# Optimization experiments

Measured on AMD Instinct MI355X. Metric: run time of the kernel, lower is better.

The kernel has to match this reference:

```python
import jax, jax.numpy as jnp
import numpy as np

B, N = 4, 2048
INPUT_DIM, KDIM, VDIM = 128, 128, 16
EMBED, V_EMBED, H = 128, 128, 8
HEAD_DIM = EMBED // H          # 16
V_HEAD_DIM = V_EMBED // H      # 16 (== VDIM, required by the torch view)
SCALING = HEAD_DIM ** -0.5


def setup_inputs() -> dict:
    key = jax.random.key(0)
    ks = jax.random.split(key, 12)
    inp = {
        "query": jax.random.normal(ks[0], (B, N, INPUT_DIM), dtype=jnp.float32),
        "key": jax.random.normal(ks[1], (B, N, KDIM), dtype=jnp.float32),
        "value": jax.random.normal(ks[2], (B, N, VDIM), dtype=jnp.float32),
        # nn.Linear weights are [out, in]; init.normal_ -> std normal
        "Wq": jax.random.normal(ks[3], (EMBED, INPUT_DIM), dtype=jnp.float32),
        "bq": jnp.zeros((EMBED,), dtype=jnp.float32),
        "Wk": jax.random.normal(ks[4], (EMBED, KDIM), dtype=jnp.float32),
        "bk": jnp.zeros((EMBED,), dtype=jnp.float32),
        "Wv": jax.random.normal(ks[5], (V_EMBED, VDIM), dtype=jnp.float32),
        "bv": jnp.zeros((V_EMBED,), dtype=jnp.float32),
        "Wo": jax.random.normal(ks[6], (V_EMBED // H, V_EMBED), dtype=jnp.float32),
        "bo": jnp.zeros((V_EMBED // H,), dtype=jnp.float32),
    }
    return inp


def reference(query, key, value, Wq, bq, Wk, bk, Wv, bv, Wo, bo):
    # projections
    q = (query @ Wq.T + bq) * SCALING                 # [B, N, EMBED]
    k = key @ Wk.T + bk                               # [B, N, EMBED]
    v = value @ Wv.T + bv                             # [B, N, V_EMBED]
    # split heads: [B, H, N, head_dim]
    q = q.reshape(B, N, H, HEAD_DIM).transpose(0, 2, 1, 3)
    k = k.reshape(B, N, H, HEAD_DIM).transpose(0, 2, 1, 3)
    v = v.reshape(B, N, H, V_HEAD_DIM).transpose(0, 2, 1, 3)
    # full NxN scores (naive attention, as in the source)
    scores = jnp.einsum("bhnd,bhmd->bhnm", q, k)      # [B, H, N, N]
    attn = jax.nn.softmax(scores, axis=-1)
    # dropout is identity in eval mode
    ctx = jnp.einsum("bhnm,bhme->bhne", attn, v)      # [B, H, N, V_HEAD_DIM]
    ctx = ctx.transpose(0, 2, 1, 3).reshape(B, N, V_EMBED)
    out = ctx @ Wo.T + bo                             # [B, N, V_EMBED // H]
    return out
```

## Files before the change

kernel.cpp:

```cpp
#include <hip/hip_runtime.h>
#include <hip/hip_bf16.h>
#include <math.h>

typedef unsigned short ushort_t;
typedef unsigned int uint_t;
typedef __bf16 bf16x8 __attribute__((ext_vector_type(8)));
typedef float f32x4 __attribute__((ext_vector_type(4)));
typedef __fp16 fp16v2 __attribute__((ext_vector_type(2)));
typedef _Float16 f16x4 __attribute__((ext_vector_type(4)));

#define NSEQ 2048
#define QSCALE 0.3606737602222409f

__device__ __forceinline__ float exp2_fast(float x) {
#if __has_builtin(__builtin_amdgcn_exp2f)
    return __builtin_amdgcn_exp2f(x);
#else
    return exp2f(x);
#endif
}

union U8 { ushort_t u[8]; bf16x8 v; uint4 q; uint_t w[4]; };
union F8 { float f[8]; float4 v4[2]; };
union H4 { fp16v2 h2[2]; f16x4 v; uint_t w[2]; };
union HV { fp16v2 h2[4]; uint4 q; };

__device__ __forceinline__ uint_t pk2(float a, float b) {
    __hip_bfloat162 h2 = __float22bfloat162_rn(make_float2(a, b));
    union { __hip_bfloat162 h; uint_t u; } cv; cv.h = h2; return cv.u;
}

__device__ __forceinline__ void split8(const F8& x, U8& hi, U8& lo) {
#pragma unroll
    for (int p = 0; p < 4; ++p) {
        const float a = x.f[2*p], b = x.f[2*p+1];
        const uint_t hw = pk2(a, b);
        hi.w[p] = hw;
        const float ha = __uint_as_float(hw << 16);
        const float hb = __uint_as_float(hw & 0xFFFF0000u);
        lo.w[p] = pk2(a - ha, b - hb);
    }
}

__global__ __launch_bounds__(256) void wpack_kernel(
    const float* __restrict__ Wq, const float* __restrict__ Wk,
    const float* __restrict__ Wo,
    ushort_t* __restrict__ wpk_hi, ushort_t* __restrict__ wpk_lo,
    ushort_t* __restrict__ wo_hi, ushort_t* __restrict__ wo_lo)
{
    const int idx = blockIdx.x * 256 + threadIdx.x;
    if (idx < 4096) {
        const int lane = idx & 63;
        const int f    = (idx >> 6) & 3;
        const int ct   = (idx >> 8) & 7;
        const int mat  = idx >> 11;
        const float* W = mat ? Wk : Wq;
        const float* src = W + (size_t)(ct * 16 + (lane & 15)) * 128
                             + f * 32 + (lane >> 4) * 8;
        F8 x; x.v4[0] = *(const float4*)src; x.v4[1] = *(const float4*)(src + 4);
        U8 hi, lo;
        split8(x, hi, lo);
        const size_t dst = (size_t)mat * 16384 + ((size_t)(ct * 4 + f) * 64 + lane) * 8;
        *(uint4*)(wpk_hi + dst) = hi.q;
        *(uint4*)(wpk_lo + dst) = lo.q;
    } else if (idx < 4352) {
        const int i2   = idx - 4096;
        const int lane = i2 & 63;
        const int f    = i2 >> 6;
        const float* src = Wo + (size_t)(lane & 15) * 128
                              + f * 32 + (lane >> 4) * 8;
        F8 x; x.v4[0] = *(const float4*)src; x.v4[1] = *(const float4*)(src + 4);
        U8 hi, lo;
        split8(x, hi, lo);
        const size_t dst = ((size_t)f * 64 + lane) * 8;
        *(uint4*)(wo_hi + dst) = hi.q;
        *(uint4*)(wo_lo + dst) = lo.q;
    }
}

__global__ __launch_bounds__(256, 2) void proj_kernel(
    const float* __restrict__ query, const float* __restrict__ key,
    const float* __restrict__ value,
    const float* __restrict__ bq, const float* __restrict__ bk,
    const float* __restrict__ Wv, const float* __restrict__ bv,
    const ushort_t* __restrict__ wpk_hi, const ushort_t* __restrict__ wpk_lo,
    ushort_t* __restrict__ q_hi, ushort_t* __restrict__ q_lo,
    ushort_t* __restrict__ k_hi, ushort_t* __restrict__ k_lo,
    ushort_t* __restrict__ vt)
{
    const int t   = threadIdx.x;
    const int w   = t >> 6;
    const int l   = t & 63;
    const int col = l & 15;
    const int g   = l >> 4;
    const int rbase = blockIdx.x * 16;
    const int b = rbase >> 11;

    const int isK    = w >> 1;
    const int cthalf = (w & 1) * 4;

    const float* X = isK ? key : query;
    const float* xrow = X + (size_t)(rbase + col) * 128 + g * 8;
    bf16x8 xh[4], xl[4];
#pragma unroll
    for (int f = 0; f < 4; ++f) {
        F8 x;
        x.v4[0] = *(const float4*)(xrow + f * 32);
        x.v4[1] = *(const float4*)(xrow + f * 32 + 4);
        U8 hi, lo;
        split8(x, hi, lo);
        xh[f] = hi.v; xl[f] = lo.v;
    }

    const float* bias = isK ? bk : bq;
    ushort_t* dhi = isK ? k_hi : q_hi;
    ushort_t* dlo = isK ? k_lo : q_lo;
    const float scale = isK ? 1.0f : QSCALE;
    const int tok = (rbase & 2047) + col;

#pragma unroll
    for (int ctl = 0; ctl < 4; ++ctl) {
        const int h = cthalf + ctl;
        bf16x8 whf[4], wlf[4];
#pragma unroll
        for (int f = 0; f < 4; ++f) {
            const size_t o = (size_t)isK * 16384
                           + ((size_t)(h * 4 + f) * 64 + l) * 8;
            whf[f] = *(const bf16x8*)(wpk_hi + o);
            wlf[f] = *(const bf16x8*)(wpk_lo + o);
        }
        const float4 b4 = *(const float4*)(bias + h * 16 + 4 * g);
        f32x4 acc = {b4.x, b4.y, b4.z, b4.w};
#pragma unroll
        for (int f = 0; f < 4; ++f) {
            acc = __builtin_amdgcn_mfma_f32_16x16x32_bf16(whf[f], xh[f], acc, 0, 0, 0);
            acc = __builtin_amdgcn_mfma_f32_16x16x32_bf16(wlf[f], xh[f], acc, 0, 0, 0);
            acc = __builtin_amdgcn_mfma_f32_16x16x32_bf16(whf[f], xl[f], acc, 0, 0, 0);
        }
        const size_t abase = ((size_t)(b * 8 + h) * NSEQ + tok) * 16 + 4 * g;
        const float a0 = acc[0]*scale, a1 = acc[1]*scale;
        const float a2 = acc[2]*scale, a3 = acc[3]*scale;
        const uint_t h01 = pk2(a0, a1), h23 = pk2(a2, a3);
        const uint_t l01 = pk2(a0 - __uint_as_float(h01 << 16),
                               a1 - __uint_as_float(h01 & 0xFFFF0000u));
        const uint_t l23 = pk2(a2 - __uint_as_float(h23 << 16),
                               a3 - __uint_as_float(h23 & 0xFFFF0000u));
        uint2 sh; sh.x = h01; sh.y = h23;
        uint2 sl; sl.x = l01; sl.y = l23;
        *(uint2*)(dhi + abase) = sh;
        *(uint2*)(dlo + abase) = sl;
    }

    const int e  = t & 127;
    const int rh = t >> 7;
    const int r0 = rbase + rh * 8;
    const float4* Wv4 = (const float4*)(Wv + (size_t)e * 16);
    const float4 wv0 = Wv4[0], wv1 = Wv4[1], wv2 = Wv4[2], wv3 = Wv4[3];
    const float bvv = bv[e];
    F8 af;
#pragma unroll
    for (int r = 0; r < 8; ++r) {
        const float4* xv4 = (const float4*)(value + (size_t)(r0 + r) * 16);
        const float4 x0 = xv4[0], x1 = xv4[1], x2 = xv4[2], x3 = xv4[3];
        float a = bvv;
        a += wv0.x*x0.x + wv0.y*x0.y + wv0.z*x0.z + wv0.w*x0.w;
        a += wv1.x*x1.x + wv1.y*x1.y + wv1.z*x1.z + wv1.w*x1.w;
        a += wv2.x*x2.x + wv2.y*x2.y + wv2.z*x2.z + wv2.w*x2.w;
        a += wv3.x*x3.x + wv3.y*x3.y + wv3.z*x3.z + wv3.w*x3.w;
        af.f[r] = a;
    }
    HV vpk;
#pragma unroll
    for (int p = 0; p < 4; ++p)
        vpk.h2[p] = __builtin_amdgcn_cvt_pkrtz(af.f[2*p], af.f[2*p+1]);
    const int hv = e >> 4, dd = e & 15;
    *(uint4*)(vt + ((size_t)(b * 8 + hv) * 16 + dd) * NSEQ + (r0 & 2047)) = vpk.q;
}

__global__ __launch_bounds__(256, 4) void attn_kernel(
    const ushort_t* __restrict__ q_hi, const ushort_t* __restrict__ q_lo,
    const ushort_t* __restrict__ k_hi, const ushort_t* __restrict__ k_lo,
    const ushort_t* __restrict__ vt, ushort_t* __restrict__ ctxb)
{
    const int t    = threadIdx.x;
    const int w    = t >> 6;
    const int l    = t & 63;
    const int col  = l & 15;
    const int g    = l >> 4;
    const int qsub = w & 1;
    const int kh   = w >> 1;

    const int id   = blockIdx.x;
    const int rest = id >> 3;
    const int bh   = (rest >> 5) * 8 + (id & 7);
    const int qbase = (rest & 31) * 64 + qsub * 32;

    __shared__ float lds_m[4][32];
    __shared__ __align__(16) float lds_o[2][2][16][16];
    __shared__ float lds_l[2][2][16];

    U8 Uz;
#pragma unroll
    for (int i = 0; i < 8; ++i) Uz.u[i] = 0;
    const bf16x8 zf = Uz.v;

    bf16x8 bq1[2], bq2[2];
#pragma unroll
    for (int s = 0; s < 2; ++s) {
        const size_t qoff = ((size_t)(bh * NSEQ + qbase + s * 16 + col)) * 16 + (g & 1) * 8;
        bq1[s] = *(const bf16x8*)(q_hi + qoff);
        const bf16x8 t2 = *(const bf16x8*)(q_lo + qoff);
        bq2[s] = (g < 2) ? t2 : zf;
    }

    const ushort_t* ksel = (g < 2) ? k_hi : k_lo;
    const ushort_t* aptr = ksel + ((size_t)bh * NSEQ + col) * 16 + (g & 1) * 8
                         + (size_t)kh * (1024 * 16);
    const ushort_t* vp = vt + ((size_t)bh * 16 + col) * NSEQ + kh * 1024;

    float m0 = -INFINITY, m1 = -INFINITY;
    const f32x4 z = {0.f, 0.f, 0.f, 0.f};
    bf16x8 pa1[2], pa2[2];
    pa1[0] = *(const bf16x8*)(aptr);
    pa2[0] = *(const bf16x8*)(aptr + 256);
    pa1[1] = *(const bf16x8*)(aptr + 512);
    pa2[1] = *(const bf16x8*)(aptr + 768);
#pragma unroll 2
    for (int kb = 0; kb < 32; ++kb) {
        const bf16x8 c1 = pa1[kb & 1], c2 = pa2[kb & 1];
        const int kn = (kb + 2) & 31;
        pa1[kb & 1] = *(const bf16x8*)(aptr + (size_t)kn * 512);
        pa2[kb & 1] = *(const bf16x8*)(aptr + (size_t)kn * 512 + 256);
        const f32x4 s1 = __builtin_amdgcn_mfma_f32_16x16x32_bf16(c1, bq1[0], z, 0, 0, 0);
        const f32x4 s2 = __builtin_amdgcn_mfma_f32_16x16x32_bf16(c2, bq1[0], z, 0, 0, 0);
        const f32x4 s3 = __builtin_amdgcn_mfma_f32_16x16x32_bf16(c1, bq1[1], z, 0, 0, 0);
        const f32x4 s4 = __builtin_amdgcn_mfma_f32_16x16x32_bf16(c2, bq1[1], z, 0, 0, 0);
        m0 = fmaxf(m0, fmaxf(fmaxf(s1[0], s1[1]), fmaxf(s1[2], s1[3])));
        m0 = fmaxf(m0, fmaxf(fmaxf(s2[0], s2[1]), fmaxf(s2[2], s2[3])));
        m1 = fmaxf(m1, fmaxf(fmaxf(s3[0], s3[1]), fmaxf(s3[2], s3[3])));
        m1 = fmaxf(m1, fmaxf(fmaxf(s4[0], s4[1]), fmaxf(s4[2], s4[3])));
    }
    m0 = fmaxf(m0, __shfl_xor(m0, 16)); m0 = fmaxf(m0, __shfl_xor(m0, 32));
    m1 = fmaxf(m1, __shfl_xor(m1, 16)); m1 = fmaxf(m1, __shfl_xor(m1, 32));
    if (l < 32) lds_m[w][l] = (l < 16) ? m0 : m1;
    __syncthreads();
    const float mf0 = fmaxf(m0, lds_m[w ^ 2][col]);
    const float mf1 = fmaxf(m1, lds_m[w ^ 2][col + 16]);
    const f32x4 zin0 = {-mf0, -mf0, -mf0, -mf0};
    const f32x4 zin1 = {-mf1, -mf1, -mf1, -mf1};

    f32x4 o0 = {0.f,0.f,0.f,0.f}, o1 = {0.f,0.f,0.f,0.f};
    float ls0 = 0.f, ls1 = 0.f;
    f16x4 pv1[2], pv2[2];
    pv1[0] = *(const f16x4*)(vp + g * 4);
    pv2[0] = *(const f16x4*)(vp + 16 + g * 4);
    pv1[1] = *(const f16x4*)(vp + 32 + g * 4);
    pv2[1] = *(const f16x4*)(vp + 48 + g * 4);

#pragma unroll 2
    for (int kb = 0; kb < 32; ++kb) {
        const bf16x8 c1 = pa1[kb & 1], c2 = pa2[kb & 1];
        const f16x4 v1 = pv1[kb & 1], v2 = pv2[kb & 1];
        const int kn = (kb + 2) & 31;
        pa1[kb & 1] = *(const bf16x8*)(aptr + (size_t)kn * 512);
        pa2[kb & 1] = *(const bf16x8*)(aptr + (size_t)kn * 512 + 256);
        pv1[kb & 1] = *(const f16x4*)(vp + kn * 32 + g * 4);
        pv2[kb & 1] = *(const f16x4*)(vp + kn * 32 + 16 + g * 4);

        {
            f32x4 st1 = __builtin_amdgcn_mfma_f32_16x16x32_bf16(c1, bq2[0], zin0, 0, 0, 0);
            st1       = __builtin_amdgcn_mfma_f32_16x16x32_bf16(c1, bq1[0], st1, 0, 0, 0);
            f32x4 st2 = __builtin_amdgcn_mfma_f32_16x16x32_bf16(c2, bq2[0], zin0, 0, 0, 0);
            st2       = __builtin_amdgcn_mfma_f32_16x16x32_bf16(c2, bq1[0], st2, 0, 0, 0);
            const float p0 = exp2_fast(st1[0]), p1 = exp2_fast(st1[1]);
            const float p2 = exp2_fast(st1[2]), p3 = exp2_fast(st1[3]);
            const float p4 = exp2_fast(st2[0]), p5 = exp2_fast(st2[1]);
            const float p6 = exp2_fast(st2[2]), p7 = exp2_fast(st2[3]);
            ls0 += ((p0 + p1) + (p2 + p3)) + ((p4 + p5) + (p6 + p7));
            H4 b1u, b2u;
            b1u.h2[0] = __builtin_amdgcn_cvt_pkrtz(p0, p1);
            b1u.h2[1] = __builtin_amdgcn_cvt_pkrtz(p2, p3);
            b2u.h2[0] = __builtin_amdgcn_cvt_pkrtz(p4, p5);
            b2u.h2[1] = __builtin_amdgcn_cvt_pkrtz(p6, p7);
            o0 = __builtin_amdgcn_mfma_f32_16x16x16f16(v1, b1u.v, o0, 0, 0, 0);
            o0 = __builtin_amdgcn_mfma_f32_16x16x16f16(v2, b2u.v, o0, 0, 0, 0);
        }
        {
            f32x4 st1 = __builtin_amdgcn_mfma_f32_16x16x32_bf16(c1, bq2[1], zin1, 0, 0, 0);
            st1       = __builtin_amdgcn_mfma_f32_16x16x32_bf16(c1, bq1[1], st1, 0, 0, 0);
            f32x4 st2 = __builtin_amdgcn_mfma_f32_16x16x32_bf16(c2, bq2[1], zin1, 0, 0, 0);
            st2       = __builtin_amdgcn_mfma_f32_16x16x32_bf16(c2, bq1[1], st2, 0, 0, 0);
            const float p0 = exp2_fast(st1[0]), p1 = exp2_fast(st1[1]);
            const float p2 = exp2_fast(st1[2]), p3 = exp2_fast(st1[3]);
            const float p4 = exp2_fast(st2[0]), p5 = exp2_fast(st2[1]);
            const float p6 = exp2_fast(st2[2]), p7 = exp2_fast(st2[3]);
            ls1 += ((p0 + p1) + (p2 + p3)) + ((p4 + p5) + (p6 + p7));
            H4 b1u, b2u;
            b1u.h2[0] = __builtin_amdgcn_cvt_pkrtz(p0, p1);
            b1u.h2[1] = __builtin_amdgcn_cvt_pkrtz(p2, p3);
            b2u.h2[0] = __builtin_amdgcn_cvt_pkrtz(p4, p5);
            b2u.h2[1] = __builtin_amdgcn_cvt_pkrtz(p6, p7);
            o1 = __builtin_amdgcn_mfma_f32_16x16x16f16(v1, b1u.v, o1, 0, 0, 0);
            o1 = __builtin_amdgcn_mfma_f32_16x16x16f16(v2, b2u.v, o1, 0, 0, 0);
        }
    }

    ls0 += __shfl_xor(ls0, 16); ls0 += __shfl_xor(ls0, 32);
    ls1 += __shfl_xor(ls1, 16); ls1 += __shfl_xor(ls1, 32);

    if (w >= 2) {
        *(f32x4*)&lds_o[w - 2][0][col][4 * g] = o0;
        *(f32x4*)&lds_o[w - 2][1][col][4 * g] = o1;
        if (l < 32) lds_l[w - 2][l >> 4][col] = (l < 16) ? ls0 : ls1;
    }
    __syncthreads();
    if (w < 2) {
        const int b = bh >> 3, h = bh & 7;
#pragma unroll
        for (int s = 0; s < 2; ++s) {
            const f32x4 ob = *(const f32x4*)&lds_o[w][s][col][4 * g];
            const f32x4 oa = s ? o1 : o0;
            const float lt = (s ? ls1 : ls0) + lds_l[w][s][col];
            const float li = 1.0f / lt;
            const float r0 = (oa[0] + ob[0]) * li;
            const float r1 = (oa[1] + ob[1]) * li;
            const float r2 = (oa[2] + ob[2]) * li;
            const float r3 = (oa[3] + ob[3]) * li;
            uint2 pkd; pkd.x = pk2(r0, r1); pkd.y = pk2(r2, r3);
            *(uint2*)(ctxb + ((size_t)(b * NSEQ + qbase + s * 16 + col)) * 128
                      + h * 16 + 4 * g) = pkd;
        }
    }
}

__global__ __launch_bounds__(64) void outproj_kernel(
    const ushort_t* __restrict__ ctxb,
    const ushort_t* __restrict__ wo_hi, const ushort_t* __restrict__ wo_lo,
    const float* __restrict__ bo, float* __restrict__ out)
{
    const int l   = threadIdx.x;
    const int col = l & 15;
    const int g   = l >> 4;
    const int row0 = blockIdx.x * 16;

    const float bval = bo[col];
    f32x4 acc = {bval, bval, bval, bval};
    const ushort_t* ar = ctxb + (size_t)(row0 + col) * 128 + g * 8;
#pragma unroll
    for (int f = 0; f < 4; ++f) {
        const bf16x8 a = *(const bf16x8*)(ar + f * 32);
        const size_t o = ((size_t)f * 64 + l) * 8;
        const bf16x8 bh_ = *(const bf16x8*)(wo_hi + o);
        const bf16x8 bl_ = *(const bf16x8*)(wo_lo + o);
        acc = __builtin_amdgcn_mfma_f32_16x16x32_bf16(a, bh_, acc, 0, 0, 0);
        acc = __builtin_amdgcn_mfma_f32_16x16x32_bf16(a, bl_, acc, 0, 0, 0);
    }
#pragma unroll
    for (int r = 0; r < 4; ++r)
        out[(size_t)(row0 + 4 * g + r) * 16 + col] = acc[r];
}

extern "C" void kernel_launch(void* const* d_in, const int* in_sizes, int n_in,
                              void* d_out, int out_size, void* d_ws, size_t ws_size,
                              hipStream_t stream)
{
    const float* query = (const float*)d_in[0];
    const float* key_  = (const float*)d_in[1];
    const float* value = (const float*)d_in[2];
    const float* Wq = (const float*)d_in[3];
    const float* bq = (const float*)d_in[4];
    const float* Wk = (const float*)d_in[5];
    const float* bk = (const float*)d_in[6];
    const float* Wv = (const float*)d_in[7];
    const float* bv = (const float*)d_in[8];
    const float* Wo = (const float*)d_in[9];
    const float* bo = (const float*)d_in[10];
    float* out = (float*)d_out;

    ushort_t* base = (ushort_t*)d_ws;
    ushort_t* q_hi = base;
    ushort_t* q_lo = base + (1u << 20);
    ushort_t* k_hi = base + (2u << 20);
    ushort_t* k_lo = base + (3u << 20);
    ushort_t* vt   = base + (4u << 20);
    ushort_t* ctxb = base + (5u << 20);
    ushort_t* wpk_hi = base + (6u << 20);
    ushort_t* wpk_lo = wpk_hi + 32768;
    ushort_t* wo_hi  = wpk_hi + 65536;
    ushort_t* wo_lo  = wo_hi + 2048;

    wpack_kernel<<<dim3(17), dim3(256), 0, stream>>>(
        Wq, Wk, Wo, wpk_hi, wpk_lo, wo_hi, wo_lo);
    proj_kernel<<<dim3(512), dim3(256), 0, stream>>>(
        query, key_, value, bq, bk, Wv, bv, wpk_hi, wpk_lo,
        q_hi, q_lo, k_hi, k_lo, vt);
    attn_kernel<<<dim3(1024), dim3(256), 0, stream>>>(
        q_hi, q_lo, k_hi, k_lo, vt, ctxb);
    outproj_kernel<<<dim3(512), dim3(64), 0, stream>>>(
        ctxb, wo_hi, wo_lo, bo, out);
}
```

Measured before the change: 135.4 us.

## Drop weight pre-pack kernel; split weights inline and widen projection grid

Removes the separate weight-packing launch. The projection and output-projection kernels now read the fp32 Wq/Wk/Wo directly and split them into bf16 hi/lo pairs in registers. The projection kernel is regridded so each wave handles one (token tile, matrix, head) triple, and the V projection moves into its own trailing blocks (2560 blocks total, occupancy hint raised to 4). This saves a kernel launch and the serialization it causes, at the cost of redundant weight loads and splitting per wave and more blocks re-reading query/key rows.

```diff
diff --git a/kernel.cpp b/kernel.cpp
--- a/kernel.cpp
+++ b/kernel.cpp
@@ -42,93 +42,57 @@
     }
 }
 
-__global__ __launch_bounds__(256) void wpack_kernel(
-    const float* __restrict__ Wq, const float* __restrict__ Wk,
-    const float* __restrict__ Wo,
-    ushort_t* __restrict__ wpk_hi, ushort_t* __restrict__ wpk_lo,
-    ushort_t* __restrict__ wo_hi, ushort_t* __restrict__ wo_lo)
-{
-    const int idx = blockIdx.x * 256 + threadIdx.x;
-    if (idx < 4096) {
-        const int lane = idx & 63;
-        const int f    = (idx >> 6) & 3;
-        const int ct   = (idx >> 8) & 7;
-        const int mat  = idx >> 11;
-        const float* W = mat ? Wk : Wq;
-        const float* src = W + (size_t)(ct * 16 + (lane & 15)) * 128
-                             + f * 32 + (lane >> 4) * 8;
-        F8 x; x.v4[0] = *(const float4*)src; x.v4[1] = *(const float4*)(src + 4);
-        U8 hi, lo;
-        split8(x, hi, lo);
-        const size_t dst = (size_t)mat * 16384 + ((size_t)(ct * 4 + f) * 64 + lane) * 8;
-        *(uint4*)(wpk_hi + dst) = hi.q;
-        *(uint4*)(wpk_lo + dst) = lo.q;
-    } else if (idx < 4352) {
-        const int i2   = idx - 4096;
-        const int lane = i2 & 63;
-        const int f    = i2 >> 6;
-        const float* src = Wo + (size_t)(lane & 15) * 128
-                              + f * 32 + (lane >> 4) * 8;
-        F8 x; x.v4[0] = *(const float4*)src; x.v4[1] = *(const float4*)(src + 4);
-        U8 hi, lo;
-        split8(x, hi, lo);
-        const size_t dst = ((size_t)f * 64 + lane) * 8;
-        *(uint4*)(wo_hi + dst) = hi.q;
-        *(uint4*)(wo_lo + dst) = lo.q;
-    }
-}
-
-__global__ __launch_bounds__(256, 2) void proj_kernel(
+__global__ __launch_bounds__(256, 4) void qkv_proj_kernel(
     const float* __restrict__ query, const float* __restrict__ key,
     const float* __restrict__ value,
-    const float* __restrict__ bq, const float* __restrict__ bk,
+    const float* __restrict__ Wq, const float* __restrict__ bq,
+    const float* __restrict__ Wk, const float* __restrict__ bk,
     const float* __restrict__ Wv, const float* __restrict__ bv,
-    const ushort_t* __restrict__ wpk_hi, const ushort_t* __restrict__ wpk_lo,
     ushort_t* __restrict__ q_hi, ushort_t* __restrict__ q_lo,
     ushort_t* __restrict__ k_hi, ushort_t* __restrict__ k_lo,
     ushort_t* __restrict__ vt)
 {
-    const int t   = threadIdx.x;
-    const int w   = t >> 6;
-    const int l   = t & 63;
-    const int col = l & 15;
-    const int g   = l >> 4;
-    const int rbase = blockIdx.x * 16;
-    const int b = rbase >> 11;
-
-    const int isK    = w >> 1;
-    const int cthalf = (w & 1) * 4;
-
-    const float* X = isK ? key : query;
-    const float* xrow = X + (size_t)(rbase + col) * 128 + g * 8;
-    bf16x8 xh[4], xl[4];
-#pragma unroll
-    for (int f = 0; f < 4; ++f) {
-        F8 x;
-        x.v4[0] = *(const float4*)(xrow + f * 32);
-        x.v4[1] = *(const float4*)(xrow + f * 32 + 4);
-        U8 hi, lo;
-        split8(x, hi, lo);
-        xh[f] = hi.v; xl[f] = lo.v;
-    }
-
-    const float* bias = isK ? bk : bq;
-    ushort_t* dhi = isK ? k_hi : q_hi;
-    ushort_t* dlo = isK ? k_lo : q_lo;
-    const float scale = isK ? 1.0f : QSCALE;
-    const int tok = (rbase & 2047) + col;
-
-#pragma unroll
-    for (int ctl = 0; ctl < 4; ++ctl) {
-        const int h = cthalf + ctl;
+    const int t = threadIdx.x;
+    if (blockIdx.x < 2048) {
+        const int w   = t >> 6;
+        const int l   = t & 63;
+        const int col = l & 15;
+        const int g   = l >> 4;
+
+        const int gw  = blockIdx.x * 4 + w;
+        const int mat = gw & 1;
+        const int h   = (gw >> 1) & 7;
+        const int T   = gw >> 4;
+        const int rbase = T * 16;
+        const int b = rbase >> 11;
+
+        const float* X = mat ? key : query;
+        const float* xrow = X + (size_t)(rbase + col) * 128 + g * 8;
+        bf16x8 xh[4], xl[4];
+#pragma unroll
+        for (int f = 0; f < 4; ++f) {
+            F8 x;
+            x.v4[0] = *(const float4*)(xrow + f * 32);
+            x.v4[1] = *(const float4*)(xrow + f * 32 + 4);
+            U8 hi, lo;
+            split8(x, hi, lo);
+            xh[f] = hi.v; xl[f] = lo.v;
+        }
+
+        const float* W = mat ? Wk : Wq;
+        const float* wrow = W + (size_t)(h * 16 + col) * 128 + g * 8;
         bf16x8 whf[4], wlf[4];
 #pragma unroll
         for (int f = 0; f < 4; ++f) {
-            const size_t o = (size_t)isK * 16384
-                           + ((size_t)(h * 4 + f) * 64 + l) * 8;
-            whf[f] = *(const bf16x8*)(wpk_hi + o);
-            wlf[f] = *(const bf16x8*)(wpk_lo + o);
-        }
+            F8 x;
+            x.v4[0] = *(const float4*)(wrow + f * 32);
+            x.v4[1] = *(const float4*)(wrow + f * 32 + 4);
+            U8 hi, lo;
+            split8(x, hi, lo);
+            whf[f] = hi.v; wlf[f] = lo.v;
+        }
+
+        const float* bias = mat ? bk : bq;
         const float4 b4 = *(const float4*)(bias + h * 16 + 4 * g);
         f32x4 acc = {b4.x, b4.y, b4.z, b4.w};
 #pragma unroll
@@ -137,6 +101,11 @@
             acc = __builtin_amdgcn_mfma_f32_16x16x32_bf16(wlf[f], xh[f], acc, 0, 0, 0);
             acc = __builtin_amdgcn_mfma_f32_16x16x32_bf16(whf[f], xl[f], acc, 0, 0, 0);
         }
+
+        ushort_t* dhi = mat ? k_hi : q_hi;
+        ushort_t* dlo = mat ? k_lo : q_lo;
+        const float scale = mat ? 1.0f : QSCALE;
+        const int tok = (rbase & 2047) + col;
         const size_t abase = ((size_t)(b * 8 + h) * NSEQ + tok) * 16 + 4 * g;
         const float a0 = acc[0]*scale, a1 = acc[1]*scale;
         const float a2 = acc[2]*scale, a3 = acc[3]*scale;
@@ -149,32 +118,34 @@
         uint2 sl; sl.x = l01; sl.y = l23;
         *(uint2*)(dhi + abase) = sh;
         *(uint2*)(dlo + abase) = sl;
-    }
-
-    const int e  = t & 127;
-    const int rh = t >> 7;
-    const int r0 = rbase + rh * 8;
-    const float4* Wv4 = (const float4*)(Wv + (size_t)e * 16);
-    const float4 wv0 = Wv4[0], wv1 = Wv4[1], wv2 = Wv4[2], wv3 = Wv4[3];
-    const float bvv = bv[e];
-    F8 af;
-#pragma unroll
-    for (int r = 0; r < 8; ++r) {
-        const float4* xv4 = (const float4*)(value + (size_t)(r0 + r) * 16);
-        const float4 x0 = xv4[0], x1 = xv4[1], x2 = xv4[2], x3 = xv4[3];
-        float a = bvv;
-        a += wv0.x*x0.x + wv0.y*x0.y + wv0.z*x0.z + wv0.w*x0.w;
-        a += wv1.x*x1.x + wv1.y*x1.y + wv1.z*x1.z + wv1.w*x1.w;
-        a += wv2.x*x2.x + wv2.y*x2.y + wv2.z*x2.z + wv2.w*x2.w;
-        a += wv3.x*x3.x + wv3.y*x3.y + wv3.z*x3.z + wv3.w*x3.w;
-        af.f[r] = a;
-    }
-    HV vpk;
-#pragma unroll
-    for (int p = 0; p < 4; ++p)
-        vpk.h2[p] = __builtin_amdgcn_cvt_pkrtz(af.f[2*p], af.f[2*p+1]);
-    const int hv = e >> 4, dd = e & 15;
-    *(uint4*)(vt + ((size_t)(b * 8 + hv) * 16 + dd) * NSEQ + (r0 & 2047)) = vpk.q;
+    } else {
+        const int rbase = (blockIdx.x - 2048) * 16;
+        const int b = rbase >> 11;
+        const int e  = t & 127;
+        const int rh = t >> 7;
+        const int r0 = rbase + rh * 8;
+        const float4* Wv4 = (const float4*)(Wv + (size_t)e * 16);
+        const float4 wv0 = Wv4[0], wv1 = Wv4[1], wv2 = Wv4[2], wv3 = Wv4[3];
+        const float bvv = bv[e];
+        F8 af;
+#pragma unroll
+        for (int r = 0; r < 8; ++r) {
+            const float4* xv4 = (const float4*)(value + (size_t)(r0 + r) * 16);
+            const float4 x0 = xv4[0], x1 = xv4[1], x2 = xv4[2], x3 = xv4[3];
+            float a = bvv;
+            a += wv0.x*x0.x + wv0.y*x0.y + wv0.z*x0.z + wv0.w*x0.w;
+            a += wv1.x*x1.x + wv1.y*x1.y + wv1.z*x1.z + wv1.w*x1.w;
+            a += wv2.x*x2.x + wv2.y*x2.y + wv2.z*x2.z + wv2.w*x2.w;
+            a += wv3.x*x3.x + wv3.y*x3.y + wv3.z*x3.z + wv3.w*x3.w;
+            af.f[r] = a;
+        }
+        HV vpk;
+#pragma unroll
+        for (int p = 0; p < 4; ++p)
+            vpk.h2[p] = __builtin_amdgcn_cvt_pkrtz(af.f[2*p], af.f[2*p+1]);
+        const int hv = e >> 4, dd = e & 15;
+        *(uint4*)(vt + ((size_t)(b * 8 + hv) * 16 + dd) * NSEQ + (r0 & 2047)) = vpk.q;
+    }
 }
 
 __global__ __launch_bounds__(256, 4) void attn_kernel(
@@ -334,8 +305,7 @@
 }
 
 __global__ __launch_bounds__(64) void outproj_kernel(
-    const ushort_t* __restrict__ ctxb,
-    const ushort_t* __restrict__ wo_hi, const ushort_t* __restrict__ wo_lo,
+    const ushort_t* __restrict__ ctxb, const float* __restrict__ Wo,
     const float* __restrict__ bo, float* __restrict__ out)
 {
     const int l   = threadIdx.x;
@@ -343,17 +313,20 @@
     const int g   = l >> 4;
     const int row0 = blockIdx.x * 16;
 
+    const float* wrow = Wo + (size_t)col * 128 + g * 8;
     const float bval = bo[col];
     f32x4 acc = {bval, bval, bval, bval};
     const ushort_t* ar = ctxb + (size_t)(row0 + col) * 128 + g * 8;
 #pragma unroll
     for (int f = 0; f < 4; ++f) {
+        F8 x;
+        x.v4[0] = *(const float4*)(wrow + f * 32);
+        x.v4[1] = *(const float4*)(wrow + f * 32 + 4);
+        U8 hi, lo;
+        split8(x, hi, lo);
         const bf16x8 a = *(const bf16x8*)(ar + f * 32);
-        const size_t o = ((size_t)f * 64 + l) * 8;
-        const bf16x8 bh_ = *(const bf16x8*)(wo_hi + o);
-        const bf16x8 bl_ = *(const bf16x8*)(wo_lo + o);
-        acc = __builtin_amdgcn_mfma_f32_16x16x32_bf16(a, bh_, acc, 0, 0, 0);
-        acc = __builtin_amdgcn_mfma_f32_16x16x32_bf16(a, bl_, acc, 0, 0, 0);
+        acc = __builtin_amdgcn_mfma_f32_16x16x32_bf16(a, hi.v, acc, 0, 0, 0);
+        acc = __builtin_amdgcn_mfma_f32_16x16x32_bf16(a, lo.v, acc, 0, 0, 0);
     }
 #pragma unroll
     for (int r = 0; r < 4; ++r)
@@ -384,18 +357,12 @@
     ushort_t* k_lo = base + (3u << 20);
     ushort_t* vt   = base + (4u << 20);
     ushort_t* ctxb = base + (5u << 20);
-    ushort_t* wpk_hi = base + (6u << 20);
-    ushort_t* wpk_lo = wpk_hi + 32768;
-    ushort_t* wo_hi  = wpk_hi + 65536;
-    ushort_t* wo_lo  = wo_hi + 2048;
-
-    wpack_kernel<<<dim3(17), dim3(256), 0, stream>>>(
-        Wq, Wk, Wo, wpk_hi, wpk_lo, wo_hi, wo_lo);
-    proj_kernel<<<dim3(512), dim3(256), 0, stream>>>(
-        query, key_, value, bq, bk, Wv, bv, wpk_hi, wpk_lo,
+
+    qkv_proj_kernel<<<dim3(2560), dim3(256), 0, stream>>>(
+        query, key_, value, Wq, bq, Wk, bk, Wv, bv,
         q_hi, q_lo, k_hi, k_lo, vt);
     attn_kernel<<<dim3(1024), dim3(256), 0, stream>>>(
         q_hi, q_lo, k_hi, k_lo, vt, ctxb);
     outproj_kernel<<<dim3(512), dim3(64), 0, stream>>>(
-        ctxb, wo_hi, wo_lo, bo, out);
-}
+        ctxb, Wo, bo, out);
+}
```

After: 150.6 us. 1.11x slower.

## Split projection and attention work across more blocks for higher parallelism

Applied to the files above, without the earlier changes.

The projection kernel now gives each wave one (matrix, head, 16-row tile) unit and runs the V projection in separate blocks, growing the grid from 512 to 2560 blocks. The attention kernel now has all four waves share one 32-query tile and each take a quarter of the keys, doubling the block count to 2048, with a four-way merge of max, sum and output through LDS. Launch bounds are raised so more blocks can be resident. The goal is better occupancy and less tail latency. The cost is more redundant Q and X loads, more reduction work through LDS, and possible register pressure from the tighter launch bounds.

```diff
diff --git a/kernel.cpp b/kernel.cpp
--- a/kernel.cpp
+++ b/kernel.cpp
@@ -78,7 +78,7 @@
     }
 }
 
-__global__ __launch_bounds__(256, 2) void proj_kernel(
+__global__ __launch_bounds__(256, 4) void qkv_proj_kernel(
     const float* __restrict__ query, const float* __restrict__ key,
     const float* __restrict__ value,
     const float* __restrict__ bq, const float* __restrict__ bk,
@@ -88,47 +88,42 @@
     ushort_t* __restrict__ k_hi, ushort_t* __restrict__ k_lo,
     ushort_t* __restrict__ vt)
 {
-    const int t   = threadIdx.x;
-    const int w   = t >> 6;
-    const int l   = t & 63;
-    const int col = l & 15;
-    const int g   = l >> 4;
-    const int rbase = blockIdx.x * 16;
-    const int b = rbase >> 11;
-
-    const int isK    = w >> 1;
-    const int cthalf = (w & 1) * 4;
-
-    const float* X = isK ? key : query;
-    const float* xrow = X + (size_t)(rbase + col) * 128 + g * 8;
-    bf16x8 xh[4], xl[4];
-#pragma unroll
-    for (int f = 0; f < 4; ++f) {
-        F8 x;
-        x.v4[0] = *(const float4*)(xrow + f * 32);
-        x.v4[1] = *(const float4*)(xrow + f * 32 + 4);
-        U8 hi, lo;
-        split8(x, hi, lo);
-        xh[f] = hi.v; xl[f] = lo.v;
-    }
-
-    const float* bias = isK ? bk : bq;
-    ushort_t* dhi = isK ? k_hi : q_hi;
-    ushort_t* dlo = isK ? k_lo : q_lo;
-    const float scale = isK ? 1.0f : QSCALE;
-    const int tok = (rbase & 2047) + col;
-
-#pragma unroll
-    for (int ctl = 0; ctl < 4; ++ctl) {
-        const int h = cthalf + ctl;
+    const int t = threadIdx.x;
+    if (blockIdx.x < 2048) {
+        const int w   = t >> 6;
+        const int l   = t & 63;
+        const int col = l & 15;
+        const int g   = l >> 4;
+
+        const int gw  = blockIdx.x * 4 + w;
+        const int mat = gw & 1;
+        const int h   = (gw >> 1) & 7;
+        const int T   = gw >> 4;
+        const int rbase = T * 16;
+        const int b = rbase >> 11;
+
+        const float* X = mat ? key : query;
+        const float* xrow = X + (size_t)(rbase + col) * 128 + g * 8;
+        bf16x8 xh[4], xl[4];
+#pragma unroll
+        for (int f = 0; f < 4; ++f) {
+            F8 x;
+            x.v4[0] = *(const float4*)(xrow + f * 32);
+            x.v4[1] = *(const float4*)(xrow + f * 32 + 4);
+            U8 hi, lo;
+            split8(x, hi, lo);
+            xh[f] = hi.v; xl[f] = lo.v;
+        }
+
         bf16x8 whf[4], wlf[4];
 #pragma unroll
         for (int f = 0; f < 4; ++f) {
-            const size_t o = (size_t)isK * 16384
-                           + ((size_t)(h * 4 + f) * 64 + l) * 8;
+            const size_t o = (size_t)mat * 16384 + ((size_t)(h * 4 + f) * 64 + l) * 8;
             whf[f] = *(const bf16x8*)(wpk_hi + o);
             wlf[f] = *(const bf16x8*)(wpk_lo + o);
         }
+
+        const float* bias = mat ? bk : bq;
         const float4 b4 = *(const float4*)(bias + h * 16 + 4 * g);
         f32x4 acc = {b4.x, b4.y, b4.z, b4.w};
 #pragma unroll
@@ -137,6 +132,11 @@
             acc = __builtin_amdgcn_mfma_f32_16x16x32_bf16(wlf[f], xh[f], acc, 0, 0, 0);
             acc = __builtin_amdgcn_mfma_f32_16x16x32_bf16(whf[f], xl[f], acc, 0, 0, 0);
         }
+
+        ushort_t* dhi = mat ? k_hi : q_hi;
+        ushort_t* dlo = mat ? k_lo : q_lo;
+        const float scale = mat ? 1.0f : QSCALE;
+        const int tok = (rbase & 2047) + col;
         const size_t abase = ((size_t)(b * 8 + h) * NSEQ + tok) * 16 + 4 * g;
         const float a0 = acc[0]*scale, a1 = acc[1]*scale;
         const float a2 = acc[2]*scale, a3 = acc[3]*scale;
@@ -149,35 +149,37 @@
         uint2 sl; sl.x = l01; sl.y = l23;
         *(uint2*)(dhi + abase) = sh;
         *(uint2*)(dlo + abase) = sl;
-    }
-
-    const int e  = t & 127;
-    const int rh = t >> 7;
-    const int r0 = rbase + rh * 8;
-    const float4* Wv4 = (const float4*)(Wv + (size_t)e * 16);
-    const float4 wv0 = Wv4[0], wv1 = Wv4[1], wv2 = Wv4[2], wv3 = Wv4[3];
-    const float bvv = bv[e];
-    F8 af;
-#pragma unroll
-    for (int r = 0; r < 8; ++r) {
-        const float4* xv4 = (const float4*)(value + (size_t)(r0 + r) * 16);
-        const float4 x0 = xv4[0], x1 = xv4[1], x2 = xv4[2], x3 = xv4[3];
-        float a = bvv;
-        a += wv0.x*x0.x + wv0.y*x0.y + wv0.z*x0.z + wv0.w*x0.w;
-        a += wv1.x*x1.x + wv1.y*x1.y + wv1.z*x1.z + wv1.w*x1.w;
-        a += wv2.x*x2.x + wv2.y*x2.y + wv2.z*x2.z + wv2.w*x2.w;
-        a += wv3.x*x3.x + wv3.y*x3.y + wv3.z*x3.z + wv3.w*x3.w;
-        af.f[r] = a;
-    }
-    HV vpk;
-#pragma unroll
-    for (int p = 0; p < 4; ++p)
-        vpk.h2[p] = __builtin_amdgcn_cvt_pkrtz(af.f[2*p], af.f[2*p+1]);
-    const int hv = e >> 4, dd = e & 15;
-    *(uint4*)(vt + ((size_t)(b * 8 + hv) * 16 + dd) * NSEQ + (r0 & 2047)) = vpk.q;
-}
-
-__global__ __launch_bounds__(256, 4) void attn_kernel(
+    } else {
+        const int rbase = (blockIdx.x - 2048) * 16;
+        const int b = rbase >> 11;
+        const int e  = t & 127;
+        const int rh = t >> 7;
+        const int r0 = rbase + rh * 8;
+        const float4* Wv4 = (const float4*)(Wv + (size_t)e * 16);
+        const float4 wv0 = Wv4[0], wv1 = Wv4[1], wv2 = Wv4[2], wv3 = Wv4[3];
+        const float bvv = bv[e];
+        F8 af;
+#pragma unroll
+        for (int r = 0; r < 8; ++r) {
+            const float4* xv4 = (const float4*)(value + (size_t)(r0 + r) * 16);
+            const float4 x0 = xv4[0], x1 = xv4[1], x2 = xv4[2], x3 = xv4[3];
+            float a = bvv;
+            a += wv0.x*x0.x + wv0.y*x0.y + wv0.z*x0.z + wv0.w*x0.w;
+            a += wv1.x*x1.x + wv1.y*x1.y + wv1.z*x1.z + wv1.w*x1.w;
+            a += wv2.x*x2.x + wv2.y*x2.y + wv2.z*x2.z + wv2.w*x2.w;
+            a += wv3.x*x3.x + wv3.y*x3.y + wv3.z*x3.z + wv3.w*x3.w;
+            af.f[r] = a;
+        }
+        HV vpk;
+#pragma unroll
+        for (int p = 0; p < 4; ++p)
+            vpk.h2[p] = __builtin_amdgcn_cvt_pkrtz(af.f[2*p], af.f[2*p+1]);
+        const int hv = e >> 4, dd = e & 15;
+        *(uint4*)(vt + ((size_t)(b * 8 + hv) * 16 + dd) * NSEQ + (r0 & 2047)) = vpk.q;
+    }
+}
+
+__global__ __launch_bounds__(256, 8) void attn_kernel(
     const ushort_t* __restrict__ q_hi, const ushort_t* __restrict__ q_lo,
     const ushort_t* __restrict__ k_hi, const ushort_t* __restrict__ k_lo,
     const ushort_t* __restrict__ vt, ushort_t* __restrict__ ctxb)
@@ -187,17 +189,15 @@
     const int l    = t & 63;
     const int col  = l & 15;
     const int g    = l >> 4;
-    const int qsub = w & 1;
-    const int kh   = w >> 1;
 
     const int id   = blockIdx.x;
     const int rest = id >> 3;
-    const int bh   = (rest >> 5) * 8 + (id & 7);
-    const int qbase = (rest & 31) * 64 + qsub * 32;
+    const int bh   = (rest >> 6) * 8 + (id & 7);
+    const int qbase = (rest & 63) * 32;
 
     __shared__ float lds_m[4][32];
-    __shared__ __align__(16) float lds_o[2][2][16][16];
-    __shared__ float lds_l[2][2][16];
+    __shared__ __align__(16) float lds_o[3][2][16][16];
+    __shared__ float lds_l[3][2][16];
 
     U8 Uz;
 #pragma unroll
@@ -215,8 +215,8 @@
 
     const ushort_t* ksel = (g < 2) ? k_hi : k_lo;
     const ushort_t* aptr = ksel + ((size_t)bh * NSEQ + col) * 16 + (g & 1) * 8
-                         + (size_t)kh * (1024 * 16);
-    const ushort_t* vp = vt + ((size_t)bh * 16 + col) * NSEQ + kh * 1024;
+                         + (size_t)w * (512 * 16);
+    const ushort_t* vp = vt + ((size_t)bh * 16 + col) * NSEQ + w * 512;
 
     float m0 = -INFINITY, m1 = -INFINITY;
     const f32x4 z = {0.f, 0.f, 0.f, 0.f};
@@ -226,9 +226,9 @@
     pa1[1] = *(const bf16x8*)(aptr + 512);
     pa2[1] = *(const bf16x8*)(aptr + 768);
 #pragma unroll 2
-    for (int kb = 0; kb < 32; ++kb) {
+    for (int kb = 0; kb < 16; ++kb) {
         const bf16x8 c1 = pa1[kb & 1], c2 = pa2[kb & 1];
-        const int kn = (kb + 2) & 31;
+        const int kn = (kb + 2) & 15;
         pa1[kb & 1] = *(const bf16x8*)(aptr + (size_t)kn * 512);
         pa2[kb & 1] = *(const bf16x8*)(aptr + (size_t)kn * 512 + 256);
         const f32x4 s1 = __builtin_amdgcn_mfma_f32_16x16x32_bf16(c1, bq1[0], z, 0, 0, 0);
@@ -244,8 +244,10 @@
     m1 = fmaxf(m1, __shfl_xor(m1, 16)); m1 = fmaxf(m1, __shfl_xor(m1, 32));
     if (l < 32) lds_m[w][l] = (l < 16) ? m0 : m1;
     __syncthreads();
-    const float mf0 = fmaxf(m0, lds_m[w ^ 2][col]);
-    const float mf1 = fmaxf(m1, lds_m[w ^ 2][col + 16]);
+    const float mf0 = fmaxf(fmaxf(lds_m[0][col],      lds_m[1][col]),
+                            fmaxf(lds_m[2][col],      lds_m[3][col]));
+    const float mf1 = fmaxf(fmaxf(lds_m[0][col + 16], lds_m[1][col + 16]),
+                            fmaxf(lds_m[2][col + 16], lds_m[3][col + 16]));
     const f32x4 zin0 = {-mf0, -mf0, -mf0, -mf0};
     const f32x4 zin1 = {-mf1, -mf1, -mf1, -mf1};
 
@@ -258,10 +260,10 @@
     pv2[1] = *(const f16x4*)(vp + 48 + g * 4);
 
 #pragma unroll 2
-    for (int kb = 0; kb < 32; ++kb) {
+    for (int kb = 0; kb < 16; ++kb) {
         const bf16x8 c1 = pa1[kb & 1], c2 = pa2[kb & 1];
         const f16x4 v1 = pv1[kb & 1], v2 = pv2[kb & 1];
-        const int kn = (kb + 2) & 31;
+        const int kn = (kb + 2) & 15;
         pa1[kb & 1] = *(const bf16x8*)(aptr + (size_t)kn * 512);
         pa2[kb & 1] = *(const bf16x8*)(aptr + (size_t)kn * 512 + 256);
         pv1[kb & 1] = *(const f16x4*)(vp + kn * 32 + g * 4);
@@ -308,25 +310,28 @@
     ls0 += __shfl_xor(ls0, 16); ls0 += __shfl_xor(ls0, 32);
     ls1 += __shfl_xor(ls1, 16); ls1 += __shfl_xor(ls1, 32);
 
-    if (w >= 2) {
-        *(f32x4*)&lds_o[w - 2][0][col][4 * g] = o0;
-        *(f32x4*)&lds_o[w - 2][1][col][4 * g] = o1;
-        if (l < 32) lds_l[w - 2][l >> 4][col] = (l < 16) ? ls0 : ls1;
+    if (w > 0) {
+        *(f32x4*)&lds_o[w - 1][0][col][4 * g] = o0;
+        *(f32x4*)&lds_o[w - 1][1][col][4 * g] = o1;
+        if (l < 32) lds_l[w - 1][l >> 4][col] = (l < 16) ? ls0 : ls1;
     }
     __syncthreads();
-    if (w < 2) {
+    if (w == 0) {
         const int b = bh >> 3, h = bh & 7;
 #pragma unroll
         for (int s = 0; s < 2; ++s) {
-            const f32x4 ob = *(const f32x4*)&lds_o[w][s][col][4 * g];
-            const f32x4 oa = s ? o1 : o0;
-            const float lt = (s ? ls1 : ls0) + lds_l[w][s][col];
+            f32x4 oa = s ? o1 : o0;
+            float lt = s ? ls1 : ls0;
+#pragma unroll
+            for (int j = 0; j < 3; ++j) {
+                const f32x4 ob = *(const f32x4*)&lds_o[j][s][col][4 * g];
+                oa[0] += ob[0]; oa[1] += ob[1]; oa[2] += ob[2]; oa[3] += ob[3];
+                lt += lds_l[j][s][col];
+            }
             const float li = 1.0f / lt;
-            const float r0 = (oa[0] + ob[0]) * li;
-            const float r1 = (oa[1] + ob[1]) * li;
-            const float r2 = (oa[2] + ob[2]) * li;
-            const float r3 = (oa[3] + ob[3]) * li;
-            uint2 pkd; pkd.x = pk2(r0, r1); pkd.y = pk2(r2, r3);
+            uint2 pkd;
+            pkd.x = pk2(oa[0] * li, oa[1] * li);
+            pkd.y = pk2(oa[2] * li, oa[3] * li);
             *(uint2*)(ctxb + ((size_t)(b * NSEQ + qbase + s * 16 + col)) * 128
                       + h * 16 + 4 * g) = pkd;
         }
@@ -391,10 +396,10 @@
 
     wpack_kernel<<<dim3(17), dim3(256), 0, stream>>>(
         Wq, Wk, Wo, wpk_hi, wpk_lo, wo_hi, wo_lo);
-    proj_kernel<<<dim3(512), dim3(256), 0, stream>>>(
+    qkv_proj_kernel<<<dim3(2560), dim3(256), 0, stream>>>(
         query, key_, value, bq, bk, Wv, bv, wpk_hi, wpk_lo,
         q_hi, q_lo, k_hi, k_lo, vt);
-    attn_kernel<<<dim3(1024), dim3(256), 0, stream>>>(
+    attn_kernel<<<dim3(2048), dim3(256), 0, stream>>>(
         q_hi, q_lo, k_hi, k_lo, vt, ctxb);
     outproj_kernel<<<dim3(512), dim3(64), 0, stream>>>(
         ctxb, wo_hi, wo_lo, bo, out);
```

Result: slower. 388.0 us (+186.7%).
